# Performance work log

Measured on AMD Instinct MI355X. Metric: run time of the kernel, lower is better.

## Reference

```python
import jax, jax.numpy as jnp
import numpy as np

IN_DIM = 512
OUT_DIM = 256


def setup_inputs() -> dict:
    key = jax.random.key(0)
    ks = jax.random.split(key, 5)
    b, n, d, o = 32, 64, IN_DIM, OUT_DIM
    lim1 = 1.0 / np.sqrt(2 * d)
    lim2 = 1.0 / np.sqrt(o)
    return {
        "x": jax.random.normal(ks[0], (b, n, d), dtype=jnp.float32),
        "W1": jax.random.uniform(ks[1], (o, 2 * d), jnp.float32, -lim1, lim1),
        "b1": jax.random.uniform(ks[2], (o,), jnp.float32, -lim1, lim1),
        "W2": jax.random.uniform(ks[3], (o, o), jnp.float32, -lim2, lim2),
        "b2": jax.random.uniform(ks[4], (o,), jnp.float32, -lim2, lim2),
    }


def reference(x, W1, b1, W2, b2):
    # x: [b, n, d]; fc1 over cat(xi, xj) == xi @ Wa.T + xj @ Wb.T + b1
    b, n, d = x.shape
    Wa, Wb = W1[:, :d], W1[:, d:]
    hi = jnp.einsum("bnd,od->bno", x, Wa)  # [b, n, o]
    hj = jnp.einsum("bnd,od->bno", x, Wb)  # [b, n, o]
    h = hi[:, :, None, :] + hj[:, None, :, :] + b1  # [b, n, n, o]
    y = jax.nn.relu(jnp.einsum("bijo,po->bijp", h, W2) + b2)  # [b, n, n, o]
    mask = ~jnp.eye(n, dtype=bool)  # zero self-pairs
    y = y * mask[None, :, :, None]
    return y.sum(axis=2)  # [b, n, o]
```

## Files before the change

### kernel.cpp

```cpp
#include <hip/hip_runtime.h>
#include <hip/hip_bf16.h>


typedef unsigned short u16;
typedef __attribute__((ext_vector_type(8))) short short8v;
typedef __attribute__((ext_vector_type(4))) float float4v;

typedef __attribute__((address_space(1))) const unsigned char* gas_ptr;
typedef __attribute__((address_space(3))) unsigned char* las_ptr;

__device__ __forceinline__ void lds_load16(const void* g, void* l) {
    __builtin_amdgcn_global_load_lds((gas_ptr)g, (las_ptr)l, 16, 0, 0);
}

__device__ __forceinline__ u16 f2bf(float f) {
    unsigned u = __float_as_uint(f);
    return (u16)((u + 0x7fffu + ((u >> 16) & 1u)) >> 16);
}

__device__ __forceinline__ short8v cvt8v(float4v a, float4v b) {
    union { u16 us[8]; short8v v; } o;
    o.us[0] = f2bf(a.x); o.us[1] = f2bf(a.y); o.us[2] = f2bf(a.z); o.us[3] = f2bf(a.w);
    o.us[4] = f2bf(b.x); o.us[5] = f2bf(b.y); o.us[6] = f2bf(b.z); o.us[7] = f2bf(b.w);
    return o.v;
}

__global__ __launch_bounds__(512) void stage1_kernel(
    const float* __restrict__ x, const float* __restrict__ W1,
    const float* __restrict__ b1, const float* __restrict__ W2,
    const float* __restrict__ b2,
    u16* __restrict__ Hb, float* __restrict__ cvec) {
    const int bid = blockIdx.x;
    const int tid = threadIdx.x;
    if (bid == 256) {
        if (tid < 256) {
            float acc = b2[tid];
            const float4v* wrow = (const float4v*)(W2 + tid * 256);
#pragma unroll 8
            for (int o4 = 0; o4 < 64; ++o4) {
                float4v wv = wrow[o4];
                float4v bv = *(const float4v*)(b1 + o4 * 4);
                acc += wv.x * bv.x + wv.y * bv.y + wv.z * bv.z + wv.w * bv.w;
            }
            cvec[tid] = acc;
        }
        return;
    }

    __shared__ __align__(16) u16 As[64 * 512];
    __shared__ __align__(16) u16 Bs[64 * 512];
    const int r0 = (bid & 31) * 64;
    const int q0 = (bid >> 5) * 64;
    const int lane = tid & 63, w = tid >> 6;

#pragma unroll 4
    for (int rr = 0; rr < 8; ++rr) {
        int row = w * 8 + rr;
        const float* sA = x + (r0 + row) * 512 + lane * 8;
        int qrow = q0 + row;
        const float* sB = W1 + (qrow & 255) * 1024 + (qrow >> 8) * 512 + lane * 8;
        float4v a0 = *(const float4v*)sA;
        float4v a1 = *(const float4v*)(sA + 4);
        float4v c0 = *(const float4v*)sB;
        float4v c1 = *(const float4v*)(sB + 4);
        int du = (lane ^ (row & 7)) * 8;
        *(short8v*)&As[row * 512 + du] = cvt8v(a0, a1);
        *(short8v*)&Bs[row * 512 + du] = cvt8v(c0, c1);
    }
    __syncthreads();

    const int wm = w >> 2, wn = w & 3;
    const int rQ = lane >> 4, rM = lane & 15;
    float4v acc[2] = {};
    for (int ks = 0; ks < 16; ++ks) {
        short8v a[2], bv;
#pragma unroll
        for (int mf = 0; mf < 2; ++mf) {
            int row = wm * 32 + mf * 16 + rM;
            int unit = row * 64 + ((ks * 4 + rQ) ^ (row & 7));
            a[mf] = *(const short8v*)((const char*)As + unit * 16);
        }
        {
            int row = wn * 16 + rM;
            int unit = row * 64 + ((ks * 4 + rQ) ^ (row & 7));
            bv = *(const short8v*)((const char*)Bs + unit * 16);
        }
#pragma unroll
        for (int mf = 0; mf < 2; ++mf)
            acc[mf] = __builtin_amdgcn_mfma_f32_16x16x32_bf16(a[mf], bv, acc[mf], 0, 0, 0);
    }

#pragma unroll
    for (int mf = 0; mf < 2; ++mf)
#pragma unroll
        for (int r = 0; r < 4; ++r) {
            int orow = r0 + wm * 32 + mf * 16 + rQ * 4 + r;
            int ocol = q0 + wn * 16 + rM;
            Hb[orow * 512 + ocol] = f2bf(acc[mf][r]);
        }
}

__global__ __launch_bounds__(256) void uvpair_kernel(
    const u16* __restrict__ Hb, const float* __restrict__ W2,
    const float* __restrict__ cvec, float* __restrict__ out) {
    __shared__ __align__(16) unsigned char smem[81920];
    u16* Hs = (u16*)smem;
    u16* Ws = (u16*)(smem + 65536);
    const int bid = blockIdx.x;
    const int b = bid & 31, pc = bid >> 5;
    const int p0 = pc * 32;
    const int tid = threadIdx.x;
    const int lane = tid & 63, w = tid >> 6;

#pragma unroll 4
    for (int rr = 0; rr < 16; ++rr) {
        int row = w * 16 + rr;
        int sc = lane ^ (row & 7);
        lds_load16(Hb + (b * 64 + row) * 512 + sc * 8, (void*)&Hs[row * 512]);
    }
#pragma unroll
    for (int rr = 0; rr < 4; ++rr) {
        int row = w * 8 + rr * 2 + (lane >> 5);
        int u = lane & 31;
        const float* s = W2 + (p0 + row) * 256 + u * 8;
        float4v c0 = *(const float4v*)s;
        float4v c1 = *(const float4v*)(s + 4);
        int du = (u ^ (row & 7)) * 8;
        *(short8v*)&Ws[row * 256 + du] = cvt8v(c0, c1);
    }
    __syncthreads();

    const int uv = w & 1, rh = w >> 1;
    const int rQ = lane >> 4, rM = lane & 15;
    float4v acc[2][2] = {};
    for (int ks = 0; ks < 8; ++ks) {
        short8v a[2], bf[2];
#pragma unroll
        for (int mf = 0; mf < 2; ++mf) {
            int row = rh * 32 + mf * 16 + rM;
            int kc = uv * 32 + ks * 4 + rQ;
            int unit = row * 64 + (kc ^ (row & 7));
            a[mf] = *(const short8v*)((const char*)Hs + unit * 16);
        }
#pragma unroll
        for (int nf = 0; nf < 2; ++nf) {
            int row = nf * 16 + rM;
            int unit = row * 32 + ((ks * 4 + rQ) ^ (row & 7));
            bf[nf] = *(const short8v*)((const char*)Ws + unit * 16);
        }
#pragma unroll
        for (int mf = 0; mf < 2; ++mf)
#pragma unroll
            for (int nf = 0; nf < 2; ++nf)
                acc[mf][nf] = __builtin_amdgcn_mfma_f32_16x16x32_bf16(
                    a[mf], bf[nf], acc[mf][nf], 0, 0, 0);
    }

    __syncthreads();
    float* Us = (float*)smem;
    float* Vs = (float*)smem + 64 * 33;
    float* dst = uv ? Vs : Us;
#pragma unroll
    for (int mf = 0; mf < 2; ++mf)
#pragma unroll
        for (int nf = 0; nf < 2; ++nf)
#pragma unroll
            for (int r = 0; r < 4; ++r)
                dst[(rh * 32 + mf * 16 + rQ * 4 + r) * 33 + nf * 16 + rM] =
                    acc[mf][nf][r];
    __syncthreads();

    const int p = tid & 31;
    const int g = tid >> 5;
    const float cv = cvec[p0 + p];
    float ufull[8], red[8];
#pragma unroll
    for (int ii = 0; ii < 8; ++ii) {
        ufull[ii] = Us[(g * 8 + ii) * 33 + p] + cv;
        red[ii] = 0.f;
    }
#pragma unroll 4
    for (int j = 0; j < 64; ++j) {
        float vs = Vs[j * 33 + p];
#pragma unroll
        for (int ii = 0; ii < 8; ++ii)
            red[ii] += fmaxf(ufull[ii] + vs, 0.f);
    }
#pragma unroll
    for (int ii = 0; ii < 8; ++ii) {
        int i = g * 8 + ii;
        red[ii] -= fmaxf(ufull[ii] + Vs[i * 33 + p], 0.f);
        out[(b * 64 + i) * 256 + p0 + p] = red[ii];
    }
}

extern "C" void kernel_launch(void* const* d_in, const int* in_sizes, int n_in,
                              void* d_out, int out_size, void* d_ws, size_t ws_size,
                              hipStream_t stream) {
    const float* x  = (const float*)d_in[0];
    const float* W1 = (const float*)d_in[1];
    const float* b1 = (const float*)d_in[2];
    const float* W2 = (const float*)d_in[3];
    const float* b2 = (const float*)d_in[4];
    float* out = (float*)d_out;

    u16* Hb = (u16*)d_ws;
    float* cvec = (float*)(Hb + 2048 * 512);

    stage1_kernel<<<257, 512, 0, stream>>>(x, W1, b1, W2, b2, Hb, cvec);
    uvpair_kernel<<<256, 256, 0, stream>>>(Hb, W2, cvec, out);
}
```

Measured before the change: 25.05 us.

## Precompose W2 with W1 halves into fused weights, compute U/V directly from x

```diff
diff --git a/kernel.cpp b/kernel.cpp
--- a/kernel.cpp
+++ b/kernel.cpp
@@ -4,6 +4,7 @@
 
 typedef unsigned short u16;
 typedef __attribute__((ext_vector_type(8))) short short8v;
+typedef __attribute__((ext_vector_type(4))) short short4v;
 typedef __attribute__((ext_vector_type(4))) float float4v;
 
 typedef __attribute__((address_space(1))) const unsigned char* gas_ptr;
@@ -25,171 +26,173 @@
     return o.v;
 }
 
-__global__ __launch_bounds__(512) void stage1_kernel(
-    const float* __restrict__ x, const float* __restrict__ W1,
-    const float* __restrict__ b1, const float* __restrict__ W2,
-    const float* __restrict__ b2,
-    u16* __restrict__ Hb, float* __restrict__ cvec) {
+__global__ __launch_bounds__(256) void prep_kernel(
+    const float* __restrict__ W1, const float* __restrict__ b1,
+    const float* __restrict__ W2, const float* __restrict__ b2,
+    u16* __restrict__ Wfb, float* __restrict__ cvec) {
     const int bid = blockIdx.x;
-    const int tid = threadIdx.x;
-    if (bid == 256) {
-        if (tid < 256) {
-            float acc = b2[tid];
-            const float4v* wrow = (const float4v*)(W2 + tid * 256);
+    const int t = threadIdx.x;
+    if (bid == 64) {
+        float acc = b2[t];
+        const float4v* wrow = (const float4v*)(W2 + t * 256);
 #pragma unroll 8
-            for (int o4 = 0; o4 < 64; ++o4) {
-                float4v wv = wrow[o4];
-                float4v bv = *(const float4v*)(b1 + o4 * 4);
-                acc += wv.x * bv.x + wv.y * bv.y + wv.z * bv.z + wv.w * bv.w;
-            }
-            cvec[tid] = acc;
-        }
+        for (int o4 = 0; o4 < 64; ++o4) {
+            float4v wv = wrow[o4];
+            float4v bv = *(const float4v*)(b1 + o4 * 4);
+            acc += wv.x * bv.x + wv.y * bv.y + wv.z * bv.z + wv.w * bv.w;
+        }
+        cvec[t] = acc;
         return;
     }
 
-    __shared__ __align__(16) u16 As[64 * 512];
-    __shared__ __align__(16) u16 Bs[64 * 512];
-    const int r0 = (bid & 31) * 64;
-    const int q0 = (bid >> 5) * 64;
-    const int lane = tid & 63, w = tid >> 6;
-
-#pragma unroll 4
+    __shared__ __align__(16) u16 As[64 * 264];
+    __shared__ __align__(16) u16 Bt[64 * 264];
+    const int qt = bid >> 3, dt = bid & 7;
+    const int q0 = qt * 64, d0 = dt * 64;
+    const int p0 = q0 & 255;
+    const int off = (q0 & 256) * 2;
+    const int lane = t & 63, w = t >> 6;
+
+#pragma unroll
     for (int rr = 0; rr < 8; ++rr) {
-        int row = w * 8 + rr;
-        const float* sA = x + (r0 + row) * 512 + lane * 8;
-        int qrow = q0 + row;
-        const float* sB = W1 + (qrow & 255) * 1024 + (qrow >> 8) * 512 + lane * 8;
-        float4v a0 = *(const float4v*)sA;
-        float4v a1 = *(const float4v*)(sA + 4);
-        float4v c0 = *(const float4v*)sB;
-        float4v c1 = *(const float4v*)(sB + 4);
-        int du = (lane ^ (row & 7)) * 8;
-        *(short8v*)&As[row * 512 + du] = cvt8v(a0, a1);
-        *(short8v*)&Bs[row * 512 + du] = cvt8v(c0, c1);
-    }
-    __syncthreads();
-
-    const int wm = w >> 2, wn = w & 3;
+        int row = w * 16 + rr * 2 + (lane >> 5);
+        int c = lane & 31;
+        const float* s = W2 + (p0 + row) * 256 + c * 8;
+        float4v a0 = *(const float4v*)s, a1 = *(const float4v*)(s + 4);
+        *(short8v*)&As[row * 264 + c * 8] = cvt8v(a0, a1);
+    }
+#pragma unroll
+    for (int kk = 0; kk < 4; ++kk) {
+        const int m = t & 15, og = t >> 4;
+        const int o0 = kk * 64 + og * 4;
+        const int d4 = m * 4;
+        float4v f0 = *(const float4v*)(W1 + (o0 + 0) * 1024 + off + d0 + d4);
+        float4v f1 = *(const float4v*)(W1 + (o0 + 1) * 1024 + off + d0 + d4);
+        float4v f2 = *(const float4v*)(W1 + (o0 + 2) * 1024 + off + d0 + d4);
+        float4v f3 = *(const float4v*)(W1 + (o0 + 3) * 1024 + off + d0 + d4);
+        const int u = o0 >> 3, sub = o0 & 7;
+#pragma unroll
+        for (int dd = 0; dd < 4; ++dd) {
+            int d = d4 + dd;
+            int usw = u ^ ((d >> 3) & 7);
+            union { u16 us[4]; short4v v; } pk;
+            pk.us[0] = f2bf(f0[dd]); pk.us[1] = f2bf(f1[dd]);
+            pk.us[2] = f2bf(f2[dd]); pk.us[3] = f2bf(f3[dd]);
+            *(short4v*)&Bt[d * 264 + usw * 8 + sub] = pk.v;
+        }
+    }
+    __syncthreads();
+
+    const int wm = w >> 1, wn = w & 1;
     const int rQ = lane >> 4, rM = lane & 15;
-    float4v acc[2] = {};
-    for (int ks = 0; ks < 16; ++ks) {
-        short8v a[2], bv;
+    float4v acc[2][2] = {};
+#pragma unroll
+    for (int ks = 0; ks < 8; ++ks) {
+        short8v a[2], bf[2];
 #pragma unroll
         for (int mf = 0; mf < 2; ++mf) {
             int row = wm * 32 + mf * 16 + rM;
-            int unit = row * 64 + ((ks * 4 + rQ) ^ (row & 7));
-            a[mf] = *(const short8v*)((const char*)As + unit * 16);
-        }
-        {
-            int row = wn * 16 + rM;
-            int unit = row * 64 + ((ks * 4 + rQ) ^ (row & 7));
-            bv = *(const short8v*)((const char*)Bs + unit * 16);
+            a[mf] = *(const short8v*)&As[row * 264 + (ks * 4 + rQ) * 8];
+        }
+#pragma unroll
+        for (int nf = 0; nf < 2; ++nf) {
+            int drow = wn * 32 + nf * 16 + rM;
+            int ku = (ks * 4 + rQ) ^ ((drow >> 3) & 7);
+            bf[nf] = *(const short8v*)&Bt[drow * 264 + ku * 8];
         }
 #pragma unroll
         for (int mf = 0; mf < 2; ++mf)
-            acc[mf] = __builtin_amdgcn_mfma_f32_16x16x32_bf16(a[mf], bv, acc[mf], 0, 0, 0);
+#pragma unroll
+            for (int nf = 0; nf < 2; ++nf)
+                acc[mf][nf] = __builtin_amdgcn_mfma_f32_16x16x32_bf16(
+                    a[mf], bf[nf], acc[mf][nf], 0, 0, 0);
     }
 
 #pragma unroll
     for (int mf = 0; mf < 2; ++mf)
 #pragma unroll
-        for (int r = 0; r < 4; ++r) {
-            int orow = r0 + wm * 32 + mf * 16 + rQ * 4 + r;
-            int ocol = q0 + wn * 16 + rM;
-            Hb[orow * 512 + ocol] = f2bf(acc[mf][r]);
-        }
-}
-
-__global__ __launch_bounds__(256) void uvpair_kernel(
-    const u16* __restrict__ Hb, const float* __restrict__ W2,
+        for (int nf = 0; nf < 2; ++nf)
+#pragma unroll
+            for (int r = 0; r < 4; ++r) {
+                int q = q0 + wm * 32 + mf * 16 + rQ * 4 + r;
+                int d = d0 + wn * 32 + nf * 16 + rM;
+                Wfb[q * 512 + d] = f2bf(acc[mf][nf][r]);
+            }
+}
+
+__global__ __launch_bounds__(512) void fused_kernel(
+    const float* __restrict__ x, const u16* __restrict__ Wfb,
     const float* __restrict__ cvec, float* __restrict__ out) {
-    __shared__ __align__(16) unsigned char smem[81920];
-    u16* Hs = (u16*)smem;
-    u16* Ws = (u16*)(smem + 65536);
+    __shared__ __align__(16) u16 smem[2 * 64 * 520];
+    u16* Xs = smem;
+    u16* Ws = smem + 64 * 520;
     const int bid = blockIdx.x;
     const int b = bid & 31, pc = bid >> 5;
     const int p0 = pc * 32;
     const int tid = threadIdx.x;
     const int lane = tid & 63, w = tid >> 6;
 
-#pragma unroll 4
-    for (int rr = 0; rr < 16; ++rr) {
-        int row = w * 16 + rr;
-        int sc = lane ^ (row & 7);
-        lds_load16(Hb + (b * 64 + row) * 512 + sc * 8, (void*)&Hs[row * 512]);
-    }
-#pragma unroll
-    for (int rr = 0; rr < 4; ++rr) {
-        int row = w * 8 + rr * 2 + (lane >> 5);
-        int u = lane & 31;
-        const float* s = W2 + (p0 + row) * 256 + u * 8;
-        float4v c0 = *(const float4v*)s;
-        float4v c1 = *(const float4v*)(s + 4);
-        int du = (u ^ (row & 7)) * 8;
-        *(short8v*)&Ws[row * 256 + du] = cvt8v(c0, c1);
+#pragma unroll
+    for (int rr = 0; rr < 8; ++rr) {
+        int row = w * 8 + rr;
+        int q = (row < 32) ? (p0 + row) : (256 + p0 + (row - 32));
+        lds_load16(Wfb + q * 512 + lane * 8, (void*)&Ws[row * 520]);
+    }
+#pragma unroll
+    for (int rr = 0; rr < 8; ++rr) {
+        int row = w * 8 + rr;
+        const float* s = x + (b * 64 + row) * 512 + lane * 8;
+        float4v a0 = *(const float4v*)s, a1 = *(const float4v*)(s + 4);
+        *(short8v*)&Xs[row * 520 + lane * 8] = cvt8v(a0, a1);
     }
     __syncthreads();
 
     const int uv = w & 1, rh = w >> 1;
     const int rQ = lane >> 4, rM = lane & 15;
-    float4v acc[2][2] = {};
-    for (int ks = 0; ks < 8; ++ks) {
-        short8v a[2], bf[2];
-#pragma unroll
-        for (int mf = 0; mf < 2; ++mf) {
-            int row = rh * 32 + mf * 16 + rM;
-            int kc = uv * 32 + ks * 4 + rQ;
-            int unit = row * 64 + (kc ^ (row & 7));
-            a[mf] = *(const short8v*)((const char*)Hs + unit * 16);
-        }
+    float4v acc[2] = {};
+#pragma unroll
+    for (int ks = 0; ks < 16; ++ks) {
+        int arow = rh * 16 + rM;
+        short8v a = *(const short8v*)&Xs[arow * 520 + (ks * 4 + rQ) * 8];
 #pragma unroll
         for (int nf = 0; nf < 2; ++nf) {
-            int row = nf * 16 + rM;
-            int unit = row * 32 + ((ks * 4 + rQ) ^ (row & 7));
-            bf[nf] = *(const short8v*)((const char*)Ws + unit * 16);
-        }
-#pragma unroll
-        for (int mf = 0; mf < 2; ++mf)
-#pragma unroll
-            for (int nf = 0; nf < 2; ++nf)
-                acc[mf][nf] = __builtin_amdgcn_mfma_f32_16x16x32_bf16(
-                    a[mf], bf[nf], acc[mf][nf], 0, 0, 0);
-    }
-
-    __syncthreads();
+            int brow = uv * 32 + nf * 16 + rM;
+            short8v bf = *(const short8v*)&Ws[brow * 520 + (ks * 4 + rQ) * 8];
+            acc[nf] = __builtin_amdgcn_mfma_f32_16x16x32_bf16(a, bf, acc[nf], 0, 0, 0);
+        }
+    }
+    __syncthreads();
+
     float* Us = (float*)smem;
-    float* Vs = (float*)smem + 64 * 33;
+    float* Vs = Us + 64 * 33;
     float* dst = uv ? Vs : Us;
 #pragma unroll
-    for (int mf = 0; mf < 2; ++mf)
-#pragma unroll
-        for (int nf = 0; nf < 2; ++nf)
-#pragma unroll
-            for (int r = 0; r < 4; ++r)
-                dst[(rh * 32 + mf * 16 + rQ * 4 + r) * 33 + nf * 16 + rM] =
-                    acc[mf][nf][r];
+    for (int nf = 0; nf < 2; ++nf)
+#pragma unroll
+        for (int r = 0; r < 4; ++r)
+            dst[(rh * 16 + rQ * 4 + r) * 33 + nf * 16 + rM] = acc[nf][r];
     __syncthreads();
 
     const int p = tid & 31;
     const int g = tid >> 5;
     const float cv = cvec[p0 + p];
-    float ufull[8], red[8];
-#pragma unroll
-    for (int ii = 0; ii < 8; ++ii) {
-        ufull[ii] = Us[(g * 8 + ii) * 33 + p] + cv;
+    float uf[4], red[4];
+#pragma unroll
+    for (int ii = 0; ii < 4; ++ii) {
+        uf[ii] = Us[(g * 4 + ii) * 33 + p] + cv;
         red[ii] = 0.f;
     }
-#pragma unroll 4
+#pragma unroll 8
     for (int j = 0; j < 64; ++j) {
         float vs = Vs[j * 33 + p];
 #pragma unroll
-        for (int ii = 0; ii < 8; ++ii)
-            red[ii] += fmaxf(ufull[ii] + vs, 0.f);
-    }
-#pragma unroll
-    for (int ii = 0; ii < 8; ++ii) {
-        int i = g * 8 + ii;
-        red[ii] -= fmaxf(ufull[ii] + Vs[i * 33 + p], 0.f);
+        for (int ii = 0; ii < 4; ++ii)
+            red[ii] += fmaxf(uf[ii] + vs, 0.f);
+    }
+#pragma unroll
+    for (int ii = 0; ii < 4; ++ii) {
+        int i = g * 4 + ii;
+        red[ii] -= fmaxf(uf[ii] + Vs[i * 33 + p], 0.f);
         out[(b * 64 + i) * 256 + p0 + p] = red[ii];
     }
 }
@@ -204,9 +207,9 @@
     const float* b2 = (const float*)d_in[4];
     float* out = (float*)d_out;
 
-    u16* Hb = (u16*)d_ws;
-    float* cvec = (float*)(Hb + 2048 * 512);
-
-    stage1_kernel<<<257, 512, 0, stream>>>(x, W1, b1, W2, b2, Hb, cvec);
-    uvpair_kernel<<<256, 256, 0, stream>>>(Hb, W2, cvec, out);
-}
+    u16* Wfb = (u16*)d_ws;
+    float* cvec = (float*)(Wfb + 512 * 512);
+
+    prep_kernel<<<65, 256, 0, stream>>>(W1, b1, W2, b2, Wfb, cvec);
+    fused_kernel<<<256, 512, 0, stream>>>(x, Wfb, cvec, out);
+}
```

Result: faster. 21.36 us (-14.7%).
